# Optimization experiments

Hardware: AMD Instinct MI355X
Metric: run time of the kernel (lower is better)

Reference implementation:

```python
import jax, jax.numpy as jnp
import numpy as np

NEG_SLOPE_ATT = 0.2   # GATConv attention LeakyReLU
NEG_SLOPE_OUT = 0.01  # F.leaky_relu_ default on bend branch


def _gat(x, edge_index, edge_attr, W, a_src, a_dst, We, a_edge, bias):
    # Single-graph PyG GATConv (heads=1, concat=False, add_self_loops=True,
    # fill_value='mean' for self-loop edge_attr, dropout inactive in eval).
    # x: [N, F], edge_index: [2, E], edge_attr: [E, ED]
    N = x.shape[0]
    E = edge_attr.shape[0]
    h = x @ W  # [N, C] projected node features
    src, dst = edge_index[0], edge_index[1]
    # self-loop edge_attr = mean of incoming edge_attr per dst node
    deg = jax.ops.segment_sum(jnp.ones((E,), x.dtype), dst, num_segments=N)
    loop_attr = jax.ops.segment_sum(edge_attr, dst, num_segments=N) / jnp.maximum(deg, 1.0)[:, None]
    sl = jnp.arange(N)
    src2 = jnp.concatenate([src, sl])
    dst2 = jnp.concatenate([dst, sl])
    ea = jnp.concatenate([edge_attr, loop_attr], axis=0)  # [E+N, ED]
    eh = ea @ We  # [E+N, C]
    alpha = (h * a_src).sum(-1)[src2] + (h * a_dst).sum(-1)[dst2] + (eh * a_edge).sum(-1)
    alpha = jax.nn.leaky_relu(alpha, NEG_SLOPE_ATT)
    # per-dst-node softmax (stable)
    amax = jax.ops.segment_max(alpha, dst2, num_segments=N)
    ex = jnp.exp(alpha - amax[dst2])
    den = jax.ops.segment_sum(ex, dst2, num_segments=N)
    coef = ex / den[dst2]
    out = jax.ops.segment_sum(coef[:, None] * h[src2], dst2, num_segments=N)
    return out + bias


def setup_inputs() -> dict:
    key = jax.random.key(0)
    B, S, n, F, C, ED = 8, 16, 256, 128, 128, 4
    N = S * n
    Eb, Es = N * 16, n * 16
    ks = jax.random.split(key, 20)
    s = 0.1
    return {
        "x": jax.random.normal(ks[0], (B, S, n, F), jnp.float32),
        "section_edge_index": jax.random.randint(ks[1], (2, Es), 0, n),
        "bend_edge_index": jax.random.randint(ks[2], (2, Eb), 0, N),
        "section_edge_attr": jax.random.normal(ks[3], (B, Es, ED), jnp.float32),
        "bend_edge_attr": jax.random.normal(ks[4], (B, Eb, ED), jnp.float32),
        "enc_W": jax.random.normal(ks[5], (ED, ED), jnp.float32) * s,
        "enc_b": jnp.zeros((ED,), jnp.float32),
        "Wb": jax.random.normal(ks[6], (F, C), jnp.float32) * s,
        "a_src_b": jax.random.normal(ks[7], (C,), jnp.float32) * s,
        "a_dst_b": jax.random.normal(ks[8], (C,), jnp.float32) * s,
        "We_b": jax.random.normal(ks[9], (ED, C), jnp.float32) * s,
        "a_edge_b": jax.random.normal(ks[10], (C,), jnp.float32) * s,
        "bias_b": jnp.zeros((C,), jnp.float32),
        "Ws": jax.random.normal(ks[11], (F, C), jnp.float32) * s,
        "a_src_s": jax.random.normal(ks[12], (C,), jnp.float32) * s,
        "a_dst_s": jax.random.normal(ks[13], (C,), jnp.float32) * s,
        "We_s": jax.random.normal(ks[14], (ED, C), jnp.float32) * s,
        "a_edge_s": jax.random.normal(ks[15], (C,), jnp.float32) * s,
        "bias_s": jnp.zeros((C,), jnp.float32),
        "fuse_w": jnp.ones((2,), jnp.float32),
    }


def reference(x, section_edge_index, bend_edge_index, section_edge_attr, bend_edge_attr,
              enc_W, enc_b, Wb, a_src_b, a_dst_b, We_b, a_edge_b, bias_b,
              Ws, a_src_s, a_dst_s, We_s, a_edge_s, bias_s, fuse_w):
    B, S, n, F = x.shape
    enc_bend = bend_edge_attr @ enc_W + enc_b      # [B, Eb, ED]
    enc_sec = section_edge_attr @ enc_W + enc_b    # [B, Es, ED]
    # bend graph: one graph per batch element over all S*n nodes
    xb = x.reshape(B, S * n, F)
    gat_b = lambda xi, ei: _gat(xi, bend_edge_index, ei, Wb, a_src_b, a_dst_b, We_b, a_edge_b, bias_b)
    xb_out = jax.nn.leaky_relu(jax.vmap(gat_b)(xb, enc_bend), NEG_SLOPE_OUT)  # [B, S*n, C]
    # section graphs: one graph per (batch, section); edge_attr shared across sections
    es = jnp.broadcast_to(enc_sec[:, None], (B, S) + enc_sec.shape[1:]).reshape(B * S, *enc_sec.shape[1:])
    gat_s = lambda xi, ei: _gat(xi, section_edge_index, ei, Ws, a_src_s, a_dst_s, We_s, a_edge_s, bias_s)
    xs_out = jax.vmap(gat_s)(x.reshape(B * S, n, F), es).reshape(B, S * n, -1)
    w = jax.nn.softmax(fuse_w)
    return w[0] * xb_out + w[1] * xs_out
```

## Files before the change

kernel.cpp:

```cpp
#include <hip/hip_runtime.h>
#include <hip/hip_bf16.h>
#include <cstdint>
#include <cstddef>

#define NEG_ATT 0.2f
#define NEG_OUT 0.01f

constexpr int Bc = 8, Sc = 16, Nn = 256, Fd = 128, Cd = 128;
constexpr int NB = Sc * Nn;
constexpr int EB = NB * 16;
constexpr int ES = Nn * 16;
constexpr int NROWS = Bc * NB;
constexpr int CAP = 80;

constexpr size_t OFF_CONSTS = 0;
constexpr size_t OFF_WTB  = 4096;
constexpr size_t OFF_WTS  = OFF_WTB + (size_t)Fd * Cd * 2;
constexpr size_t OFF_HBP  = OFF_WTS + (size_t)Fd * Cd * 2;
constexpr size_t OFF_HSP  = OFF_HBP + (size_t)NROWS * 64 * 4;
constexpr size_t OFF_SSB  = OFF_HSP + (size_t)NROWS * 64 * 4;
constexpr size_t OFF_SDB  = OFF_SSB + (size_t)NROWS * 4;
constexpr size_t OFF_SSS  = OFF_SDB + (size_t)NROWS * 4;
constexpr size_t OFF_SDS  = OFF_SSS + (size_t)NROWS * 4;
constexpr size_t OFF_AEB  = OFF_SDS + (size_t)NROWS * 4;
constexpr size_t OFF_AES  = OFF_AEB + (size_t)Bc * EB * 4;
constexpr size_t OFF_ELLB = OFF_AES + (size_t)Bc * ES * 4;
constexpr size_t OFF_ELLS = OFF_ELLB + (size_t)NB * CAP * 4;
constexpr size_t OFF_FILB = OFF_ELLS + (size_t)Nn * CAP * 4;
constexpr size_t OFF_FILS = OFF_FILB + (size_t)NB * 4;
constexpr int ZERO_U32 = NB + Nn;


typedef short bf16x8 __attribute__((ext_vector_type(8)));
typedef float f32x4 __attribute__((ext_vector_type(4)));
#if defined(__has_builtin)
#if __has_builtin(__builtin_amdgcn_fdot2_f32_bf16)
#define HAS_DOT2BF 1
typedef __bf16 bf16x2 __attribute__((ext_vector_type(2)));
#endif
#endif

__device__ inline unsigned short f2bf(float f) {
  unsigned int u = __float_as_uint(f);
  u += 0x7fffu + ((u >> 16) & 1u);
  return (unsigned short)(u >> 16);
}
__device__ inline float lrelu(float x, float s) { return x > 0.f ? x : x * s; }
__device__ inline float bflo(unsigned int u) { return __uint_as_float(u << 16); }
__device__ inline float bfhi(unsigned int u) { return __uint_as_float(u & 0xffff0000u); }
__device__ inline float wave_dot128(const float* Wrow, const float* a, int lane) {
  float2 wv = *(const float2*)(Wrow + 2 * lane);
  float2 av = *(const float2*)(a + 2 * lane);
  float p = wv.x * av.x + wv.y * av.y;
  for (int off = 32; off; off >>= 1) p += __shfl_xor(p, off);
  return p;
}
__device__ inline void edge_fma(unsigned int u, uint4 v, float& o0, float& o1) {
#ifdef HAS_DOT2BF
  o0 = __builtin_amdgcn_fdot2_f32_bf16(__builtin_bit_cast(bf16x2, u),
                                       __builtin_bit_cast(bf16x2, v.y), o0, false);
  o1 = __builtin_amdgcn_fdot2_f32_bf16(__builtin_bit_cast(bf16x2, u),
                                       __builtin_bit_cast(bf16x2, v.z), o1, false);
#else
  float c = __uint_as_float(v.w);
  o0 += c * bflo(u); o1 += c * bfhi(u);
#endif
}

__global__ __launch_bounds__(256) void k_setup(
    const float* Wb, const float* a_src_b, const float* a_dst_b,
    const float* Ws, const float* a_src_s, const float* a_dst_s,
    const float* We_b, const float* a_edge_b,
    const float* We_s, const float* a_edge_s,
    const float* fuse_w, const float* enc_W, const float* enc_b,
    float* consts, unsigned short* wtb, unsigned short* wts, unsigned int* fill_region) {
  int blk = blockIdx.x, t = threadIdx.x;
  if (blk < 128) {
    int tid = blk * 256 + t;
    int which = tid >> 14, idx = tid & 16383;
    int c = idx >> 7, k = idx & 127;
    const float* W = which ? Ws : Wb;
    unsigned short* o = which ? wts : wtb;
    o[c * 128 + k] = f2bf(W[k * 128 + c]);
  } else if (blk < 160) {
    int wave = t >> 6, lane = t & 63;
    int gw = (blk - 128) * 4 + wave;
    int base = gw * 4;
    int v = base >> 7;
    const float* W = (v < 2) ? Wb : Ws;
    const float* a = (v == 0) ? a_src_b : (v == 1) ? a_dst_b : (v == 2) ? a_src_s : a_dst_s;
#pragma unroll
    for (int k = 0; k < 4; ++k) {
      int idx = base + k, f = idx & 127;
      float p = wave_dot128(W + f * 128, a, lane);
      if (lane == 0) consts[16 + v * 128 + f] = p;
    }
  } else if (blk == 160) {
    int wave = t >> 6, lane = t & 63;
    float pb = wave_dot128(We_b + wave * 128, a_edge_b, lane);
    float ps = wave_dot128(We_s + wave * 128, a_edge_s, lane);
    if (lane == 0) { consts[2 + wave] = pb; consts[6 + wave] = ps; }
    if (t == 0) {
      float f0 = fuse_w[0], f1 = fuse_w[1];
      float m = fmaxf(f0, f1);
      float e0 = __expf(f0 - m), e1 = __expf(f1 - m);
      consts[0] = e0 / (e0 + e1);
      consts[1] = e1 / (e0 + e1);
    }
  } else if (blk == 161) {
    if (t < 16) consts[544 + t] = enc_W[t];
    else if (t < 20) consts[544 + t] = enc_b[t - 16];
  } else {
    int zid = (blk - 162) * 256 + t;
    for (int z = zid; z < ZERO_U32; z += 2 * 256) fill_region[z] = 0;
  }
}

constexpr int GEMM_BLKS = NROWS / 64;
constexpr int ENC_BLKS  = (Bc * (EB + ES)) / 256;
constexpr int SCAT_BLKS = (EB + ES + 255) / 256;

__global__ __launch_bounds__(256) void k_work(
    const float* x, const float* consts,
    const unsigned short* wtb, const unsigned short* wts,
    unsigned int* hbp, unsigned int* hsp,
    float* ssb, float* sdb, float* sss, float* sds,
    const float* battr, const float* sattr, float* aeb, float* aes,
    const int* bsrc, const int* bdst, const int* ssrcA, const int* sdst,
    int* filb, int* fils, unsigned int* ellb, unsigned int* ells) {
  int blk = blockIdx.x, t = threadIdx.x;
  if (blk < GEMM_BLKS) {
    int wave = t >> 6, lane = t & 63;
    int m0 = blk * 64 + wave * 16;
    int r = lane & 15, kg = lane >> 4;
    f32x4 accB[8], accS[8];
#pragma unroll
    for (int i = 0; i < 8; ++i) { accB[i] = (f32x4){0,0,0,0}; accS[i] = (f32x4){0,0,0,0}; }
    float p0 = 0.f, p1 = 0.f, p2 = 0.f, p3 = 0.f;
    const float* wa = consts + 16;
#pragma unroll
    for (int ks = 0; ks < 4; ++ks) {
      int wo = ks * 32 + kg * 8;
      const float* xrow = x + (size_t)(m0 + r) * 128 + wo;
      float4 xa = *(const float4*)xrow;
      float4 xc = *(const float4*)(xrow + 4);
      float4 w0a = *(const float4*)(wa + 0 * 128 + wo), w0b = *(const float4*)(wa + 0 * 128 + wo + 4);
      float4 w1a = *(const float4*)(wa + 1 * 128 + wo), w1b = *(const float4*)(wa + 1 * 128 + wo + 4);
      float4 w2a = *(const float4*)(wa + 2 * 128 + wo), w2b = *(const float4*)(wa + 2 * 128 + wo + 4);
      float4 w3a = *(const float4*)(wa + 3 * 128 + wo), w3b = *(const float4*)(wa + 3 * 128 + wo + 4);
      p0 += xa.x*w0a.x + xa.y*w0a.y + xa.z*w0a.z + xa.w*w0a.w
          + xc.x*w0b.x + xc.y*w0b.y + xc.z*w0b.z + xc.w*w0b.w;
      p1 += xa.x*w1a.x + xa.y*w1a.y + xa.z*w1a.z + xa.w*w1a.w
          + xc.x*w1b.x + xc.y*w1b.y + xc.z*w1b.z + xc.w*w1b.w;
      p2 += xa.x*w2a.x + xa.y*w2a.y + xa.z*w2a.z + xa.w*w2a.w
          + xc.x*w2b.x + xc.y*w2b.y + xc.z*w2b.z + xc.w*w2b.w;
      p3 += xa.x*w3a.x + xa.y*w3a.y + xa.z*w3a.z + xa.w*w3a.w
          + xc.x*w3b.x + xc.y*w3b.y + xc.z*w3b.z + xc.w*w3b.w;
      bf16x8 a;
      a[0] = (short)f2bf(xa.x); a[1] = (short)f2bf(xa.y);
      a[2] = (short)f2bf(xa.z); a[3] = (short)f2bf(xa.w);
      a[4] = (short)f2bf(xc.x); a[5] = (short)f2bf(xc.y);
      a[6] = (short)f2bf(xc.z); a[7] = (short)f2bf(xc.w);
#pragma unroll
      for (int cb = 0; cb < 8; ++cb) {
        bf16x8 bb = *(const bf16x8*)(wtb + (size_t)(cb * 16 + r) * 128 + wo);
        accB[cb] = __builtin_amdgcn_mfma_f32_16x16x32_bf16(a, bb, accB[cb], 0, 0, 0);
        bf16x8 bs = *(const bf16x8*)(wts + (size_t)(cb * 16 + r) * 128 + wo);
        accS[cb] = __builtin_amdgcn_mfma_f32_16x16x32_bf16(a, bs, accS[cb], 0, 0, 0);
      }
    }
    p0 += __shfl_xor(p0, 16); p0 += __shfl_xor(p0, 32);
    p1 += __shfl_xor(p1, 16); p1 += __shfl_xor(p1, 32);
    p2 += __shfl_xor(p2, 16); p2 += __shfl_xor(p2, 32);
    p3 += __shfl_xor(p3, 16); p3 += __shfl_xor(p3, 32);
    if (lane < 16) {
      int row = m0 + lane;
      ssb[row] = p0; sdb[row] = p1; sss[row] = p2; sds[row] = p3;
    }
#pragma unroll
    for (int cb = 0; cb < 4; ++cb)
#pragma unroll
      for (int i = 0; i < 4; ++i) {
        size_t idx = (size_t)(m0 + kg * 4 + i) * 64 + cb * 16 + r;
        hbp[idx] = (unsigned int)f2bf(accB[cb][i]) | ((unsigned int)f2bf(accB[cb + 4][i]) << 16);
        hsp[idx] = (unsigned int)f2bf(accS[cb][i]) | ((unsigned int)f2bf(accS[cb + 4][i]) << 16);
      }
  } else if (blk < GEMM_BLKS + ENC_BLKS) {
    int idx = (blk - GEMM_BLKS) * 256 + t;
    const float* encW = consts + 544;
    bool isB = idx < Bc * EB;
    const float* attr = isB ? battr : sattr;
    const float* wae = consts + (isB ? 2 : 6);
    float* dst = isB ? aeb : aes;
    int id2 = isB ? idx : idx - Bc * EB;
    float4 at = *(const float4*)(attr + (size_t)id2 * 4);
    float e0 = encW[16] + at.x * encW[0] + at.y * encW[4] + at.z * encW[8]  + at.w * encW[12];
    float e1 = encW[17] + at.x * encW[1] + at.y * encW[5] + at.z * encW[9]  + at.w * encW[13];
    float e2 = encW[18] + at.x * encW[2] + at.y * encW[6] + at.z * encW[10] + at.w * encW[14];
    float e3 = encW[19] + at.x * encW[3] + at.y * encW[7] + at.z * encW[11] + at.w * encW[15];
    dst[id2] = e0 * wae[0] + e1 * wae[1] + e2 * wae[2] + e3 * wae[3];
  } else {
    int tid = (blk - GEMM_BLKS - ENC_BLKS) * 256 + t;
    if (tid < EB) {
      int d = bdst[tid];
      int slot = atomicAdd(&filb[d], 1);
      if (slot < CAP) ellb[(size_t)d * CAP + slot] = ((unsigned int)bsrc[tid] << 16) | (unsigned int)tid;
    } else if (tid < EB + ES) {
      int e = tid - EB;
      int d = sdst[e];
      int slot = atomicAdd(&fils[d], 1);
      if (slot < CAP) ells[(size_t)d * CAP + slot] = ((unsigned int)ssrcA[e] << 16) | (unsigned int)e;
    }
  }
}

__global__ __launch_bounds__(256) void k_gather(
    const float* ssb, const float* sdb, const float* aeb,
    const int* filb, const unsigned int* ellb, const unsigned int* hbp, const float* bias_b,
    const float* sss, const float* sds, const float* aes,
    const int* fils, const unsigned int* ells, const unsigned int* hsp, const float* bias_s,
    const float* consts, float* out) {
  __shared__ uint4 lds[4][128];
  int wg = blockIdx.x;
  int wave = threadIdx.x >> 6, lane = threadIdx.x & 63;
  int b = wg & 7;
  int i = ((wg >> 3) << 2) + wave;
  int wid = (b << 12) + i;
  int il = i & 255;
  int rowBase = wid - il;

  float oB0 = 0.f, oB1 = 0.f, oS0 = 0.f, oS1 = 0.f;

  int degB = filb[i];  if (degB > CAP) degB = CAP;
  int degS = fils[il]; if (degS > CAP) degS = CAP;
  const float* ssrcBb = ssb + ((size_t)b << 12);
  const float* ssrcGs = sss + rowBase;
  const float* aeBb = aeb + (size_t)b * EB;
  const float* aeBs = aes + (size_t)b * ES;
  const unsigned int* hBb = hbp + (((size_t)b << 12) << 6);
  const unsigned int* hGs = hsp + ((size_t)rowBase << 6);
  const unsigned int* ellBr = ellb + (size_t)i * CAP;
  const unsigned int* ellSr = ells + (size_t)il * CAP;
  unsigned int uSelfB = hbp[((size_t)wid << 6) + lane];
  unsigned int uSelfS = hsp[((size_t)wid << 6) + lane];
  float sdB = sdb[wid], sdS = sds[wid];
  float ssSelfB = ssrcBb[i], ssSelfS = ssrcGs[il];

  uint4* ldsw = lds[wave];

  if (degB <= 64 && degS <= 64) {
    bool vB = lane < degB, vS = lane < degS;
    unsigned int evB = vB ? ellBr[lane] : 0u;
    unsigned int evS = vS ? ellSr[lane] : 0u;
    int sB = evB >> 16, sS = evS >> 16;
    int eB = evB & 0xffffu, eS = evS & 0xffffu;
    float aevB = vB ? aeBb[eB] : 0.f;
    float aevS = vS ? aeBs[eS] : 0.f;
    float xsB = ssrcBb[sB];
    float xsS = ssrcGs[sS];

    float cB = vB ? __expf(lrelu(xsB + sdB + aevB, NEG_ATT)) : 0.f;
    float cS2 = vS ? __expf(lrelu(xsS + sdS + aevS, NEG_ATT)) : 0.f;

    float asumB = aevB, asumS = aevS, seB = cB, seS = cS2;
    for (int off = 32; off; off >>= 1) {
      asumB += __shfl_xor(asumB, off);
      asumS += __shfl_xor(asumS, off);
      seB += __shfl_xor(seB, off);
      seS += __shfl_xor(seS, off);
    }
    float aSB = lrelu(ssSelfB + sdB + asumB / (float)(degB > 0 ? degB : 1), NEG_ATT);
    float aSS = lrelu(ssSelfS + sdS + asumS / (float)(degS > 0 ? degS : 1), NEG_ATT);
    float eSB = __expf(aSB), eSS = __expf(aSS);
    float invB = 1.f / (seB + eSB);
    float invS = 1.f / (seS + eSS);

    {
      float cnB = cB * invB, cnS = cS2 * invS;
      unsigned int cb16 = (unsigned int)f2bf(cnB);
      unsigned int cs16 = (unsigned int)f2bf(cnS);
      uint4 slotB, slotS;
      slotB.x = (unsigned int)sB << 8; slotB.y = cb16; slotB.z = cb16 << 16; slotB.w = __float_as_uint(cnB);
      slotS.x = (unsigned int)sS << 8; slotS.y = cs16; slotS.z = cs16 << 16; slotS.w = __float_as_uint(cnS);
      ldsw[lane] = slotB;
      ldsw[64 + lane] = slotS;
    }

    const char* hBc = (const char*)hBb;
    const char* hGc = (const char*)hGs;
    int lb4 = lane * 4;
    int j = 0;
    for (; j + 4 <= degB; j += 4) {
      uint4 v0 = ldsw[j], v1 = ldsw[j+1], v2 = ldsw[j+2], v3 = ldsw[j+3];
      unsigned int u0 = *(const unsigned int*)(hBc + v0.x + lb4);
      unsigned int u1 = *(const unsigned int*)(hBc + v1.x + lb4);
      unsigned int u2 = *(const unsigned int*)(hBc + v2.x + lb4);
      unsigned int u3 = *(const unsigned int*)(hBc + v3.x + lb4);
      edge_fma(u0, v0, oB0, oB1); edge_fma(u1, v1, oB0, oB1);
      edge_fma(u2, v2, oB0, oB1); edge_fma(u3, v3, oB0, oB1);
    }
    for (; j < degB; ++j) {
      uint4 v = ldsw[j];
      unsigned int u = *(const unsigned int*)(hBc + v.x + lb4);
      edge_fma(u, v, oB0, oB1);
    }
    j = 0;
    for (; j + 4 <= degS; j += 4) {
      uint4 v0 = ldsw[64+j], v1 = ldsw[64+j+1], v2 = ldsw[64+j+2], v3 = ldsw[64+j+3];
      unsigned int u0 = *(const unsigned int*)(hGc + v0.x + lb4);
      unsigned int u1 = *(const unsigned int*)(hGc + v1.x + lb4);
      unsigned int u2 = *(const unsigned int*)(hGc + v2.x + lb4);
      unsigned int u3 = *(const unsigned int*)(hGc + v3.x + lb4);
      edge_fma(u0, v0, oS0, oS1); edge_fma(u1, v1, oS0, oS1);
      edge_fma(u2, v2, oS0, oS1); edge_fma(u3, v3, oS0, oS1);
    }
    for (; j < degS; ++j) {
      uint4 v = ldsw[64+j];
      unsigned int u = *(const unsigned int*)(hGc + v.x + lb4);
      edge_fma(u, v, oS0, oS1);
    }
    float cSelfB = eSB * invB;
    oB0 += cSelfB * bflo(uSelfB); oB1 += cSelfB * bfhi(uSelfB);
    float cSelfS = eSS * invS;
    oS0 += cSelfS * bflo(uSelfS); oS1 += cSelfS * bfhi(uSelfS);
  } else {
    float mB, invB, aSB, mS, invS, aSS;
    {
      float asum = 0.f;
      for (int p = lane; p < degB; p += 64) asum += aeBb[ellBr[p] & 0xffffu];
      for (int off = 32; off; off >>= 1) asum += __shfl_xor(asum, off);
      aSB = lrelu(ssSelfB + sdB + asum / (float)(degB > 0 ? degB : 1), NEG_ATT);
      mB = aSB;
      for (int p = lane; p < degB; p += 64) {
        unsigned int v = ellBr[p];
        mB = fmaxf(mB, lrelu(ssrcBb[v >> 16] + sdB + aeBb[v & 0xffffu], NEG_ATT));
      }
      for (int off = 32; off; off >>= 1) mB = fmaxf(mB, __shfl_xor(mB, off));
      float se = 0.f;
      for (int p = lane; p < degB; p += 64) {
        unsigned int v = ellBr[p];
        se += __expf(lrelu(ssrcBb[v >> 16] + sdB + aeBb[v & 0xffffu], NEG_ATT) - mB);
      }
      for (int off = 32; off; off >>= 1) se += __shfl_xor(se, off);
      se += __expf(aSB - mB);
      invB = 1.f / se;
      for (int j = 0; j < degB; ++j) {
        unsigned int v = ellBr[j];
        int s = v >> 16;
        float c = __expf(lrelu(ssrcBb[s] + sdB + aeBb[v & 0xffffu], NEG_ATT) - mB) * invB;
        unsigned int u = (hBb + ((size_t)s << 6))[lane];
        oB0 += c * bflo(u); oB1 += c * bfhi(u);
      }
      float cSelfB = __expf(aSB - mB) * invB;
      oB0 += cSelfB * bflo(uSelfB); oB1 += cSelfB * bfhi(uSelfB);
    }
    {
      float asum = 0.f;
      for (int p = lane; p < degS; p += 64) asum += aeBs[ellSr[p] & 0xffffu];
      for (int off = 32; off; off >>= 1) asum += __shfl_xor(asum, off);
      aSS = lrelu(ssSelfS + sdS + asum / (float)(degS > 0 ? degS : 1), NEG_ATT);
      mS = aSS;
      for (int p = lane; p < degS; p += 64) {
        unsigned int v = ellSr[p];
        mS = fmaxf(mS, lrelu(ssrcGs[v >> 16] + sdS + aeBs[v & 0xffffu], NEG_ATT));
      }
      for (int off = 32; off; off >>= 1) mS = fmaxf(mS, __shfl_xor(mS, off));
      float se = 0.f;
      for (int p = lane; p < degS; p += 64) {
        unsigned int v = ellSr[p];
        se += __expf(lrelu(ssrcGs[v >> 16] + sdS + aeBs[v & 0xffffu], NEG_ATT) - mS);
      }
      for (int off = 32; off; off >>= 1) se += __shfl_xor(se, off);
      se += __expf(aSS - mS);
      invS = 1.f / se;
      for (int j = 0; j < degS; ++j) {
        unsigned int v = ellSr[j];
        int s = v >> 16;
        float c = __expf(lrelu(ssrcGs[s] + sdS + aeBs[v & 0xffffu], NEG_ATT) - mS) * invS;
        unsigned int u = (hGs + ((size_t)s << 6))[lane];
        oS0 += c * bflo(u); oS1 += c * bfhi(u);
      }
      float cSelfS = __expf(aSS - mS) * invS;
      oS0 += cSelfS * bflo(uSelfS); oS1 += cSelfS * bfhi(uSelfS);
    }
  }

  float w0 = consts[0], w1 = consts[1];
  size_t o = (size_t)wid << 7;
  out[o + lane]      = w0 * lrelu(oB0 + bias_b[lane], NEG_OUT)      + w1 * (oS0 + bias_s[lane]);
  out[o + 64 + lane] = w0 * lrelu(oB1 + bias_b[lane + 64], NEG_OUT) + w1 * (oS1 + bias_s[lane + 64]);
}

extern "C" void kernel_launch(void* const* d_in, const int* in_sizes, int n_in,
                              void* d_out, int out_size, void* d_ws, size_t ws_size,
                              hipStream_t stream) {
  (void)in_sizes; (void)n_in; (void)out_size; (void)ws_size;
  const float* x        = (const float*)d_in[0];
  const int*   sec_ei   = (const int*)d_in[1];
  const int*   bend_ei  = (const int*)d_in[2];
  const float* sec_attr = (const float*)d_in[3];
  const float* bend_attr= (const float*)d_in[4];
  const float* enc_W    = (const float*)d_in[5];
  const float* enc_b    = (const float*)d_in[6];
  const float* Wb       = (const float*)d_in[7];
  const float* a_src_b  = (const float*)d_in[8];
  const float* a_dst_b  = (const float*)d_in[9];
  const float* We_b     = (const float*)d_in[10];
  const float* a_edge_b = (const float*)d_in[11];
  const float* bias_b   = (const float*)d_in[12];
  const float* Ws       = (const float*)d_in[13];
  const float* a_src_s  = (const float*)d_in[14];
  const float* a_dst_s  = (const float*)d_in[15];
  const float* We_s     = (const float*)d_in[16];
  const float* a_edge_s = (const float*)d_in[17];
  const float* bias_s   = (const float*)d_in[18];
  const float* fuse_w   = (const float*)d_in[19];
  float* out = (float*)d_out;

  char* ws = (char*)d_ws;
  float* consts = (float*)(ws + OFF_CONSTS);
  unsigned short* wtb = (unsigned short*)(ws + OFF_WTB);
  unsigned short* wts = (unsigned short*)(ws + OFF_WTS);
  unsigned int* hbp = (unsigned int*)(ws + OFF_HBP);
  unsigned int* hsp = (unsigned int*)(ws + OFF_HSP);
  float* ssb = (float*)(ws + OFF_SSB);
  float* sdb = (float*)(ws + OFF_SDB);
  float* sss = (float*)(ws + OFF_SSS);
  float* sds = (float*)(ws + OFF_SDS);
  float* aeb = (float*)(ws + OFF_AEB);
  float* aes = (float*)(ws + OFF_AES);
  unsigned int* ellb = (unsigned int*)(ws + OFF_ELLB);
  unsigned int* ells = (unsigned int*)(ws + OFF_ELLS);
  int* filb = (int*)(ws + OFF_FILB);
  int* fils = (int*)(ws + OFF_FILS);
  unsigned int* fill_region = (unsigned int*)(ws + OFF_FILB);

  const int* bend_src = bend_ei;
  const int* bend_dst = bend_ei + EB;
  const int* sec_src  = sec_ei;
  const int* sec_dst  = sec_ei + ES;

  k_setup<<<164, 256, 0, stream>>>(Wb, a_src_b, a_dst_b, Ws, a_src_s, a_dst_s,
                                   We_b, a_edge_b, We_s, a_edge_s, fuse_w,
                                   enc_W, enc_b, consts, wtb, wts, fill_region);

  k_work<<<GEMM_BLKS + ENC_BLKS + SCAT_BLKS, 256, 0, stream>>>(
      x, consts, wtb, wts, hbp, hsp, ssb, sdb, sss, sds,
      bend_attr, sec_attr, aeb, aes,
      bend_src, bend_dst, sec_src, sec_dst,
      filb, fils, ellb, ells);

  k_gather<<<NROWS / 4, 256, 0, stream>>>(ssb, sdb, aeb, filb, ellb, hbp, bias_b,
                                          sss, sds, aes, fils, ells, hsp, bias_s,
                                          consts, out);
}
```

Baseline: 69.79 us.

## Gather four edges per wave iteration with 16-byte loads per lane

The fast-path neighbour aggregation is restructured so each wave handles four edges per iteration. Each edge is split across 16 lanes, and each lane loads a 16-byte chunk of the bf16 feature row, replacing the old loop where every lane loaded 4 bytes for one edge at a time. The aim is to cut the serial gather iterations and load instructions and to keep more independent memory requests in flight. The cost is a cross-lane shuffle reduction at the end and more accumulator registers. The LDS slot shrinks to 8 bytes and carries an fp32 coefficient, which drops the bf16 fdot2 path, and the output is written as float4 from one lane group.

After: 72.49 us. 3.9% more time.

```diff
diff --git a/kernel.cpp b/kernel.cpp
--- a/kernel.cpp
+++ b/kernel.cpp
@@ -33,12 +33,6 @@
 
 typedef short bf16x8 __attribute__((ext_vector_type(8)));
 typedef float f32x4 __attribute__((ext_vector_type(4)));
-#if defined(__has_builtin)
-#if __has_builtin(__builtin_amdgcn_fdot2_f32_bf16)
-#define HAS_DOT2BF 1
-typedef __bf16 bf16x2 __attribute__((ext_vector_type(2)));
-#endif
-#endif
 
 __device__ inline unsigned short f2bf(float f) {
   unsigned int u = __float_as_uint(f);
@@ -54,17 +48,6 @@
   float p = wv.x * av.x + wv.y * av.y;
   for (int off = 32; off; off >>= 1) p += __shfl_xor(p, off);
   return p;
-}
-__device__ inline void edge_fma(unsigned int u, uint4 v, float& o0, float& o1) {
-#ifdef HAS_DOT2BF
-  o0 = __builtin_amdgcn_fdot2_f32_bf16(__builtin_bit_cast(bf16x2, u),
-                                       __builtin_bit_cast(bf16x2, v.y), o0, false);
-  o1 = __builtin_amdgcn_fdot2_f32_bf16(__builtin_bit_cast(bf16x2, u),
-                                       __builtin_bit_cast(bf16x2, v.z), o1, false);
-#else
-  float c = __uint_as_float(v.w);
-  o0 += c * bflo(u); o1 += c * bfhi(u);
-#endif
 }
 
 __global__ __launch_bounds__(256) void k_setup(
@@ -220,7 +203,7 @@
     const float* sss, const float* sds, const float* aes,
     const int* fils, const unsigned int* ells, const unsigned int* hsp, const float* bias_s,
     const float* consts, float* out) {
-  __shared__ uint4 lds[4][128];
+  __shared__ unsigned long long lds[4][128];
   int wg = blockIdx.x;
   int wave = threadIdx.x >> 6, lane = threadIdx.x & 63;
   int b = wg & 7;
@@ -228,8 +211,6 @@
   int wid = (b << 12) + i;
   int il = i & 255;
   int rowBase = wid - il;
-
-  float oB0 = 0.f, oB1 = 0.f, oS0 = 0.f, oS1 = 0.f;
 
   int degB = filb[i];  if (degB > CAP) degB = CAP;
   int degS = fils[il]; if (degS > CAP) degS = CAP;
@@ -241,12 +222,12 @@
   const unsigned int* hGs = hsp + ((size_t)rowBase << 6);
   const unsigned int* ellBr = ellb + (size_t)i * CAP;
   const unsigned int* ellSr = ells + (size_t)il * CAP;
-  unsigned int uSelfB = hbp[((size_t)wid << 6) + lane];
-  unsigned int uSelfS = hsp[((size_t)wid << 6) + lane];
   float sdB = sdb[wid], sdS = sds[wid];
   float ssSelfB = ssrcBb[i], ssSelfS = ssrcGs[il];
 
-  uint4* ldsw = lds[wave];
+  unsigned long long* ldsw = lds[wave];
+  float w0 = consts[0], w1 = consts[1];
+  size_t o = (size_t)wid << 7;
 
   if (degB <= 64 && degS <= 64) {
     bool vB = lane < degB, vS = lane < degS;
@@ -275,55 +256,77 @@
     float invB = 1.f / (seB + eSB);
     float invS = 1.f / (seS + eSS);
 
-    {
-      float cnB = cB * invB, cnS = cS2 * invS;
-      unsigned int cb16 = (unsigned int)f2bf(cnB);
-      unsigned int cs16 = (unsigned int)f2bf(cnS);
-      uint4 slotB, slotS;
-      slotB.x = (unsigned int)sB << 8; slotB.y = cb16; slotB.z = cb16 << 16; slotB.w = __float_as_uint(cnB);
-      slotS.x = (unsigned int)sS << 8; slotS.y = cs16; slotS.z = cs16 << 16; slotS.w = __float_as_uint(cnS);
-      ldsw[lane] = slotB;
-      ldsw[64 + lane] = slotS;
-    }
-
+    ldsw[lane]      = ((unsigned long long)__float_as_uint(cB * invB) << 32) | ((unsigned int)sB << 8);
+    ldsw[64 + lane] = ((unsigned long long)__float_as_uint(cS2 * invS) << 32) | ((unsigned int)sS << 8);
+
+    int g = lane >> 4, q = lane & 15;
+    int qb = q * 16;
     const char* hBc = (const char*)hBb;
     const char* hGc = (const char*)hGs;
-    int lb4 = lane * 4;
-    int j = 0;
-    for (; j + 4 <= degB; j += 4) {
-      uint4 v0 = ldsw[j], v1 = ldsw[j+1], v2 = ldsw[j+2], v3 = ldsw[j+3];
-      unsigned int u0 = *(const unsigned int*)(hBc + v0.x + lb4);
-      unsigned int u1 = *(const unsigned int*)(hBc + v1.x + lb4);
-      unsigned int u2 = *(const unsigned int*)(hBc + v2.x + lb4);
-      unsigned int u3 = *(const unsigned int*)(hBc + v3.x + lb4);
-      edge_fma(u0, v0, oB0, oB1); edge_fma(u1, v1, oB0, oB1);
-      edge_fma(u2, v2, oB0, oB1); edge_fma(u3, v3, oB0, oB1);
-    }
-    for (; j < degB; ++j) {
-      uint4 v = ldsw[j];
-      unsigned int u = *(const unsigned int*)(hBc + v.x + lb4);
-      edge_fma(u, v, oB0, oB1);
-    }
-    j = 0;
-    for (; j + 4 <= degS; j += 4) {
-      uint4 v0 = ldsw[64+j], v1 = ldsw[64+j+1], v2 = ldsw[64+j+2], v3 = ldsw[64+j+3];
-      unsigned int u0 = *(const unsigned int*)(hGc + v0.x + lb4);
-      unsigned int u1 = *(const unsigned int*)(hGc + v1.x + lb4);
-      unsigned int u2 = *(const unsigned int*)(hGc + v2.x + lb4);
-      unsigned int u3 = *(const unsigned int*)(hGc + v3.x + lb4);
-      edge_fma(u0, v0, oS0, oS1); edge_fma(u1, v1, oS0, oS1);
-      edge_fma(u2, v2, oS0, oS1); edge_fma(u3, v3, oS0, oS1);
-    }
-    for (; j < degS; ++j) {
-      uint4 v = ldsw[64+j];
-      unsigned int u = *(const unsigned int*)(hGc + v.x + lb4);
-      edge_fma(u, v, oS0, oS1);
-    }
-    float cSelfB = eSB * invB;
-    oB0 += cSelfB * bflo(uSelfB); oB1 += cSelfB * bfhi(uSelfB);
-    float cSelfS = eSS * invS;
-    oS0 += cSelfS * bflo(uSelfS); oS1 += cSelfS * bfhi(uSelfS);
+    float bLo0=0.f,bLo1=0.f,bLo2=0.f,bLo3=0.f, bHi0=0.f,bHi1=0.f,bHi2=0.f,bHi3=0.f;
+    float sLo0=0.f,sLo1=0.f,sLo2=0.f,sLo3=0.f, sHi0=0.f,sHi1=0.f,sHi2=0.f,sHi3=0.f;
+    for (int j = 0; j < degB; j += 4) {
+      unsigned long long v = ldsw[j + g];
+      uint4 u = *(const uint4*)(hBc + (unsigned int)v + qb);
+      float c = __uint_as_float((unsigned int)(v >> 32));
+      bLo0 += c * bflo(u.x); bHi0 += c * bfhi(u.x);
+      bLo1 += c * bflo(u.y); bHi1 += c * bfhi(u.y);
+      bLo2 += c * bflo(u.z); bHi2 += c * bfhi(u.z);
+      bLo3 += c * bflo(u.w); bHi3 += c * bfhi(u.w);
+    }
+    for (int j = 0; j < degS; j += 4) {
+      unsigned long long v = ldsw[64 + j + g];
+      uint4 u = *(const uint4*)(hGc + (unsigned int)v + qb);
+      float c = __uint_as_float((unsigned int)(v >> 32));
+      sLo0 += c * bflo(u.x); sHi0 += c * bfhi(u.x);
+      sLo1 += c * bflo(u.y); sHi1 += c * bfhi(u.y);
+      sLo2 += c * bflo(u.z); sHi2 += c * bfhi(u.z);
+      sLo3 += c * bflo(u.w); sHi3 += c * bfhi(u.w);
+    }
+    if (g == 0) {
+      float cfb = eSB * invB, cfs = eSS * invS;
+      uint4 ub = *(const uint4*)((const char*)hbp + ((size_t)wid << 8) + qb);
+      uint4 us = *(const uint4*)((const char*)hsp + ((size_t)wid << 8) + qb);
+      bLo0 += cfb * bflo(ub.x); bHi0 += cfb * bfhi(ub.x);
+      bLo1 += cfb * bflo(ub.y); bHi1 += cfb * bfhi(ub.y);
+      bLo2 += cfb * bflo(ub.z); bHi2 += cfb * bfhi(ub.z);
+      bLo3 += cfb * bflo(ub.w); bHi3 += cfb * bfhi(ub.w);
+      sLo0 += cfs * bflo(us.x); sHi0 += cfs * bfhi(us.x);
+      sLo1 += cfs * bflo(us.y); sHi1 += cfs * bfhi(us.y);
+      sLo2 += cfs * bflo(us.z); sHi2 += cfs * bfhi(us.z);
+      sLo3 += cfs * bflo(us.w); sHi3 += cfs * bfhi(us.w);
+    }
+    for (int off = 16; off <= 32; off <<= 1) {
+      bLo0 += __shfl_xor(bLo0, off); bLo1 += __shfl_xor(bLo1, off);
+      bLo2 += __shfl_xor(bLo2, off); bLo3 += __shfl_xor(bLo3, off);
+      bHi0 += __shfl_xor(bHi0, off); bHi1 += __shfl_xor(bHi1, off);
+      bHi2 += __shfl_xor(bHi2, off); bHi3 += __shfl_xor(bHi3, off);
+      sLo0 += __shfl_xor(sLo0, off); sLo1 += __shfl_xor(sLo1, off);
+      sLo2 += __shfl_xor(sLo2, off); sLo3 += __shfl_xor(sLo3, off);
+      sHi0 += __shfl_xor(sHi0, off); sHi1 += __shfl_xor(sHi1, off);
+      sHi2 += __shfl_xor(sHi2, off); sHi3 += __shfl_xor(sHi3, off);
+    }
+    if (g == 0) {
+      float4 bbL = *(const float4*)(bias_b + 4 * q);
+      float4 bbH = *(const float4*)(bias_b + 64 + 4 * q);
+      float4 bsL = *(const float4*)(bias_s + 4 * q);
+      float4 bsH = *(const float4*)(bias_s + 64 + 4 * q);
+      float4 r0, r1;
+      r0.x = w0 * lrelu(bLo0 + bbL.x, NEG_OUT) + w1 * (sLo0 + bsL.x);
+      r0.y = w0 * lrelu(bLo1 + bbL.y, NEG_OUT) + w1 * (sLo1 + bsL.y);
+      r0.z = w0 * lrelu(bLo2 + bbL.z, NEG_OUT) + w1 * (sLo2 + bsL.z);
+      r0.w = w0 * lrelu(bLo3 + bbL.w, NEG_OUT) + w1 * (sLo3 + bsL.w);
+      r1.x = w0 * lrelu(bHi0 + bbH.x, NEG_OUT) + w1 * (sHi0 + bsH.x);
+      r1.y = w0 * lrelu(bHi1 + bbH.y, NEG_OUT) + w1 * (sHi1 + bsH.y);
+      r1.z = w0 * lrelu(bHi2 + bbH.z, NEG_OUT) + w1 * (sHi2 + bsH.z);
+      r1.w = w0 * lrelu(bHi3 + bbH.w, NEG_OUT) + w1 * (sHi3 + bsH.w);
+      *(float4*)(out + o + 4 * q) = r0;
+      *(float4*)(out + o + 64 + 4 * q) = r1;
+    }
   } else {
+    float oB0 = 0.f, oB1 = 0.f, oS0 = 0.f, oS1 = 0.f;
+    unsigned int uSelfB = hbp[((size_t)wid << 6) + lane];
+    unsigned int uSelfS = hsp[((size_t)wid << 6) + lane];
     float mB, invB, aSB, mS, invS, aSS;
     {
       float asum = 0.f;
@@ -383,12 +386,9 @@
       float cSelfS = __expf(aSS - mS) * invS;
       oS0 += cSelfS * bflo(uSelfS); oS1 += cSelfS * bfhi(uSelfS);
     }
+    out[o + lane]      = w0 * lrelu(oB0 + bias_b[lane], NEG_OUT)      + w1 * (oS0 + bias_s[lane]);
+    out[o + 64 + lane] = w0 * lrelu(oB1 + bias_b[lane + 64], NEG_OUT) + w1 * (oS1 + bias_s[lane + 64]);
   }
-
-  float w0 = consts[0], w1 = consts[1];
-  size_t o = (size_t)wid << 7;
-  out[o + lane]      = w0 * lrelu(oB0 + bias_b[lane], NEG_OUT)      + w1 * (oS0 + bias_s[lane]);
-  out[o + 64 + lane] = w0 * lrelu(oB1 + bias_b[lane + 64], NEG_OUT) + w1 * (oS1 + bias_s[lane + 64]);
 }
 
 extern "C" void kernel_launch(void* const* d_in, const int* in_sizes, int n_in,
```

## Split bend and section aggregation across separate waves per node

Applied to the files above, without the earlier changes.

The gather kernel now gives each destination node two waves, one for the bend graph and one for the section graph, where before a single wave handled both. The section wave passes its partial result to the bend wave through LDS behind a block barrier, and the bend wave writes the fused output. The grid doubles to NROWS/2 blocks. The aim is more parallelism and shorter per-wave dependency chains for latency-bound gathers, at the cost of twice as many waves, a __syncthreads, and uneven work between the two waves of a node.

Measured after the change: 75.27 us. 1.08x slower.

```diff
diff --git a/kernel.cpp b/kernel.cpp
--- a/kernel.cpp
+++ b/kernel.cpp
@@ -220,175 +220,123 @@
     const float* sss, const float* sds, const float* aes,
     const int* fils, const unsigned int* ells, const unsigned int* hsp, const float* bias_s,
     const float* consts, float* out) {
-  __shared__ uint4 lds[4][128];
+  __shared__ uint4 slots[4][64];
+  __shared__ float cmb[2][128];
   int wg = blockIdx.x;
-  int wave = threadIdx.x >> 6, lane = threadIdx.x & 63;
+  int w = threadIdx.x >> 6, lane = threadIdx.x & 63;
   int b = wg & 7;
-  int i = ((wg >> 3) << 2) + wave;
+  int nl = w >> 1, ph = w & 1;
+  int i = ((wg >> 3) << 1) + nl;
   int wid = (b << 12) + i;
   int il = i & 255;
   int rowBase = wid - il;
 
-  float oB0 = 0.f, oB1 = 0.f, oS0 = 0.f, oS1 = 0.f;
-
-  int degB = filb[i];  if (degB > CAP) degB = CAP;
-  int degS = fils[il]; if (degS > CAP) degS = CAP;
-  const float* ssrcBb = ssb + ((size_t)b << 12);
-  const float* ssrcGs = sss + rowBase;
-  const float* aeBb = aeb + (size_t)b * EB;
-  const float* aeBs = aes + (size_t)b * ES;
-  const unsigned int* hBb = hbp + (((size_t)b << 12) << 6);
-  const unsigned int* hGs = hsp + ((size_t)rowBase << 6);
-  const unsigned int* ellBr = ellb + (size_t)i * CAP;
-  const unsigned int* ellSr = ells + (size_t)il * CAP;
-  unsigned int uSelfB = hbp[((size_t)wid << 6) + lane];
-  unsigned int uSelfS = hsp[((size_t)wid << 6) + lane];
-  float sdB = sdb[wid], sdS = sds[wid];
-  float ssSelfB = ssrcBb[i], ssSelfS = ssrcGs[il];
-
-  uint4* ldsw = lds[wave];
-
-  if (degB <= 64 && degS <= 64) {
-    bool vB = lane < degB, vS = lane < degS;
-    unsigned int evB = vB ? ellBr[lane] : 0u;
-    unsigned int evS = vS ? ellSr[lane] : 0u;
-    int sB = evB >> 16, sS = evS >> 16;
-    int eB = evB & 0xffffu, eS = evS & 0xffffu;
-    float aevB = vB ? aeBb[eB] : 0.f;
-    float aevS = vS ? aeBs[eS] : 0.f;
-    float xsB = ssrcBb[sB];
-    float xsS = ssrcGs[sS];
-
-    float cB = vB ? __expf(lrelu(xsB + sdB + aevB, NEG_ATT)) : 0.f;
-    float cS2 = vS ? __expf(lrelu(xsS + sdS + aevS, NEG_ATT)) : 0.f;
-
-    float asumB = aevB, asumS = aevS, seB = cB, seS = cS2;
+  float o0 = 0.f, o1 = 0.f;
+
+  const float* ssrc; const float* aeArr; const unsigned int* hB; const unsigned int* ellR;
+  int deg; float sd, ssSelf; int selfIdx;
+  if (ph == 0) {
+    deg = filb[i];  if (deg > CAP) deg = CAP;
+    ssrc = ssb + ((size_t)b << 12);
+    aeArr = aeb + (size_t)b * EB;
+    hB = hbp + (((size_t)b << 12) << 6);
+    ellR = ellb + (size_t)i * CAP;
+    sd = sdb[wid]; selfIdx = i;
+  } else {
+    deg = fils[il]; if (deg > CAP) deg = CAP;
+    ssrc = sss + rowBase;
+    aeArr = aes + (size_t)b * ES;
+    hB = hsp + ((size_t)rowBase << 6);
+    ellR = ells + (size_t)il * CAP;
+    sd = sds[wid]; selfIdx = il;
+  }
+  ssSelf = ssrc[selfIdx];
+  unsigned int uSelf = (ph == 0 ? hbp : hsp)[((size_t)wid << 6) + lane];
+  uint4* sl = slots[w];
+
+  if (deg <= 64) {
+    bool v = lane < deg;
+    unsigned int ev = v ? ellR[lane] : 0u;
+    int s = ev >> 16;
+    int e = ev & 0xffffu;
+    float aev = v ? aeArr[e] : 0.f;
+    float xs = ssrc[s];
+
+    float c = v ? __expf(lrelu(xs + sd + aev, NEG_ATT)) : 0.f;
+    float asum = aev, se = c;
     for (int off = 32; off; off >>= 1) {
-      asumB += __shfl_xor(asumB, off);
-      asumS += __shfl_xor(asumS, off);
-      seB += __shfl_xor(seB, off);
-      seS += __shfl_xor(seS, off);
-    }
-    float aSB = lrelu(ssSelfB + sdB + asumB / (float)(degB > 0 ? degB : 1), NEG_ATT);
-    float aSS = lrelu(ssSelfS + sdS + asumS / (float)(degS > 0 ? degS : 1), NEG_ATT);
-    float eSB = __expf(aSB), eSS = __expf(aSS);
-    float invB = 1.f / (seB + eSB);
-    float invS = 1.f / (seS + eSS);
-
+      asum += __shfl_xor(asum, off);
+      se += __shfl_xor(se, off);
+    }
+    float aS = lrelu(ssSelf + sd + asum / (float)(deg > 0 ? deg : 1), NEG_ATT);
+    float eS = __expf(aS);
+    float inv = 1.f / (se + eS);
+    float cn = c * inv;
     {
-      float cnB = cB * invB, cnS = cS2 * invS;
-      unsigned int cb16 = (unsigned int)f2bf(cnB);
-      unsigned int cs16 = (unsigned int)f2bf(cnS);
-      uint4 slotB, slotS;
-      slotB.x = (unsigned int)sB << 8; slotB.y = cb16; slotB.z = cb16 << 16; slotB.w = __float_as_uint(cnB);
-      slotS.x = (unsigned int)sS << 8; slotS.y = cs16; slotS.z = cs16 << 16; slotS.w = __float_as_uint(cnS);
-      ldsw[lane] = slotB;
-      ldsw[64 + lane] = slotS;
-    }
-
-    const char* hBc = (const char*)hBb;
-    const char* hGc = (const char*)hGs;
+      unsigned int c16 = (unsigned int)f2bf(cn);
+      uint4 slot;
+      slot.x = (unsigned int)s << 8; slot.y = c16; slot.z = c16 << 16; slot.w = __float_as_uint(cn);
+      sl[lane] = slot;
+    }
+    const char* hc = (const char*)hB;
     int lb4 = lane * 4;
     int j = 0;
-    for (; j + 4 <= degB; j += 4) {
-      uint4 v0 = ldsw[j], v1 = ldsw[j+1], v2 = ldsw[j+2], v3 = ldsw[j+3];
-      unsigned int u0 = *(const unsigned int*)(hBc + v0.x + lb4);
-      unsigned int u1 = *(const unsigned int*)(hBc + v1.x + lb4);
-      unsigned int u2 = *(const unsigned int*)(hBc + v2.x + lb4);
-      unsigned int u3 = *(const unsigned int*)(hBc + v3.x + lb4);
-      edge_fma(u0, v0, oB0, oB1); edge_fma(u1, v1, oB0, oB1);
-      edge_fma(u2, v2, oB0, oB1); edge_fma(u3, v3, oB0, oB1);
-    }
-    for (; j < degB; ++j) {
-      uint4 v = ldsw[j];
-      unsigned int u = *(const unsigned int*)(hBc + v.x + lb4);
-      edge_fma(u, v, oB0, oB1);
-    }
-    j = 0;
-    for (; j + 4 <= degS; j += 4) {
-      uint4 v0 = ldsw[64+j], v1 = ldsw[64+j+1], v2 = ldsw[64+j+2], v3 = ldsw[64+j+3];
-      unsigned int u0 = *(const unsigned int*)(hGc + v0.x + lb4);
-      unsigned int u1 = *(const unsigned int*)(hGc + v1.x + lb4);
-      unsigned int u2 = *(const unsigned int*)(hGc + v2.x + lb4);
-      unsigned int u3 = *(const unsigned int*)(hGc + v3.x + lb4);
-      edge_fma(u0, v0, oS0, oS1); edge_fma(u1, v1, oS0, oS1);
-      edge_fma(u2, v2, oS0, oS1); edge_fma(u3, v3, oS0, oS1);
-    }
-    for (; j < degS; ++j) {
-      uint4 v = ldsw[64+j];
-      unsigned int u = *(const unsigned int*)(hGc + v.x + lb4);
-      edge_fma(u, v, oS0, oS1);
-    }
-    float cSelfB = eSB * invB;
-    oB0 += cSelfB * bflo(uSelfB); oB1 += cSelfB * bfhi(uSelfB);
-    float cSelfS = eSS * invS;
-    oS0 += cSelfS * bflo(uSelfS); oS1 += cSelfS * bfhi(uSelfS);
+    for (; j + 4 <= deg; j += 4) {
+      uint4 v0 = sl[j], v1 = sl[j+1], v2 = sl[j+2], v3 = sl[j+3];
+      unsigned int u0 = *(const unsigned int*)(hc + v0.x + lb4);
+      unsigned int u1 = *(const unsigned int*)(hc + v1.x + lb4);
+      unsigned int u2 = *(const unsigned int*)(hc + v2.x + lb4);
+      unsigned int u3 = *(const unsigned int*)(hc + v3.x + lb4);
+      edge_fma(u0, v0, o0, o1); edge_fma(u1, v1, o0, o1);
+      edge_fma(u2, v2, o0, o1); edge_fma(u3, v3, o0, o1);
+    }
+    for (; j < deg; ++j) {
+      uint4 vv = sl[j];
+      unsigned int u = *(const unsigned int*)(hc + vv.x + lb4);
+      edge_fma(u, vv, o0, o1);
+    }
+    float cSelf = eS * inv;
+    o0 += cSelf * bflo(uSelf); o1 += cSelf * bfhi(uSelf);
   } else {
-    float mB, invB, aSB, mS, invS, aSS;
-    {
-      float asum = 0.f;
-      for (int p = lane; p < degB; p += 64) asum += aeBb[ellBr[p] & 0xffffu];
-      for (int off = 32; off; off >>= 1) asum += __shfl_xor(asum, off);
-      aSB = lrelu(ssSelfB + sdB + asum / (float)(degB > 0 ? degB : 1), NEG_ATT);
-      mB = aSB;
-      for (int p = lane; p < degB; p += 64) {
-        unsigned int v = ellBr[p];
-        mB = fmaxf(mB, lrelu(ssrcBb[v >> 16] + sdB + aeBb[v & 0xffffu], NEG_ATT));
-      }
-      for (int off = 32; off; off >>= 1) mB = fmaxf(mB, __shfl_xor(mB, off));
-      float se = 0.f;
-      for (int p = lane; p < degB; p += 64) {
-        unsigned int v = ellBr[p];
-        se += __expf(lrelu(ssrcBb[v >> 16] + sdB + aeBb[v & 0xffffu], NEG_ATT) - mB);
-      }
-      for (int off = 32; off; off >>= 1) se += __shfl_xor(se, off);
-      se += __expf(aSB - mB);
-      invB = 1.f / se;
-      for (int j = 0; j < degB; ++j) {
-        unsigned int v = ellBr[j];
-        int s = v >> 16;
-        float c = __expf(lrelu(ssrcBb[s] + sdB + aeBb[v & 0xffffu], NEG_ATT) - mB) * invB;
-        unsigned int u = (hBb + ((size_t)s << 6))[lane];
-        oB0 += c * bflo(u); oB1 += c * bfhi(u);
-      }
-      float cSelfB = __expf(aSB - mB) * invB;
-      oB0 += cSelfB * bflo(uSelfB); oB1 += cSelfB * bfhi(uSelfB);
-    }
-    {
-      float asum = 0.f;
-      for (int p = lane; p < degS; p += 64) asum += aeBs[ellSr[p] & 0xffffu];
-      for (int off = 32; off; off >>= 1) asum += __shfl_xor(asum, off);
-      aSS = lrelu(ssSelfS + sdS + asum / (float)(degS > 0 ? degS : 1), NEG_ATT);
-      mS = aSS;
-      for (int p = lane; p < degS; p += 64) {
-        unsigned int v = ellSr[p];
-        mS = fmaxf(mS, lrelu(ssrcGs[v >> 16] + sdS + aeBs[v & 0xffffu], NEG_ATT));
-      }
-      for (int off = 32; off; off >>= 1) mS = fmaxf(mS, __shfl_xor(mS, off));
-      float se = 0.f;
-      for (int p = lane; p < degS; p += 64) {
-        unsigned int v = ellSr[p];
-        se += __expf(lrelu(ssrcGs[v >> 16] + sdS + aeBs[v & 0xffffu], NEG_ATT) - mS);
-      }
-      for (int off = 32; off; off >>= 1) se += __shfl_xor(se, off);
-      se += __expf(aSS - mS);
-      invS = 1.f / se;
-      for (int j = 0; j < degS; ++j) {
-        unsigned int v = ellSr[j];
-        int s = v >> 16;
-        float c = __expf(lrelu(ssrcGs[s] + sdS + aeBs[v & 0xffffu], NEG_ATT) - mS) * invS;
-        unsigned int u = (hGs + ((size_t)s << 6))[lane];
-        oS0 += c * bflo(u); oS1 += c * bfhi(u);
-      }
-      float cSelfS = __expf(aSS - mS) * invS;
-      oS0 += cSelfS * bflo(uSelfS); oS1 += cSelfS * bfhi(uSelfS);
-    }
+    float asum = 0.f;
+    for (int p = lane; p < deg; p += 64) asum += aeArr[ellR[p] & 0xffffu];
+    for (int off = 32; off; off >>= 1) asum += __shfl_xor(asum, off);
+    float aS = lrelu(ssSelf + sd + asum / (float)(deg > 0 ? deg : 1), NEG_ATT);
+    float m = aS;
+    for (int p = lane; p < deg; p += 64) {
+      unsigned int v = ellR[p];
+      m = fmaxf(m, lrelu(ssrc[v >> 16] + sd + aeArr[v & 0xffffu], NEG_ATT));
+    }
+    for (int off = 32; off; off >>= 1) m = fmaxf(m, __shfl_xor(m, off));
+    float se = 0.f;
+    for (int p = lane; p < deg; p += 64) {
+      unsigned int v = ellR[p];
+      se += __expf(lrelu(ssrc[v >> 16] + sd + aeArr[v & 0xffffu], NEG_ATT) - m);
+    }
+    for (int off = 32; off; off >>= 1) se += __shfl_xor(se, off);
+    se += __expf(aS - m);
+    float inv = 1.f / se;
+    for (int j = 0; j < deg; ++j) {
+      unsigned int v = ellR[j];
+      int s = v >> 16;
+      float c = __expf(lrelu(ssrc[s] + sd + aeArr[v & 0xffffu], NEG_ATT) - m) * inv;
+      unsigned int u = (hB + ((size_t)s << 6))[lane];
+      o0 += c * bflo(u); o1 += c * bfhi(u);
+    }
+    float cSelf = __expf(aS - m) * inv;
+    o0 += cSelf * bflo(uSelf); o1 += cSelf * bfhi(uSelf);
   }
 
-  float w0 = consts[0], w1 = consts[1];
-  size_t o = (size_t)wid << 7;
-  out[o + lane]      = w0 * lrelu(oB0 + bias_b[lane], NEG_OUT)      + w1 * (oS0 + bias_s[lane]);
-  out[o + 64 + lane] = w0 * lrelu(oB1 + bias_b[lane + 64], NEG_OUT) + w1 * (oS1 + bias_s[lane + 64]);
+  if (ph == 1) { cmb[nl][lane] = o0; cmb[nl][64 + lane] = o1; }
+  __syncthreads();
+  if (ph == 0) {
+    float w0 = consts[0], w1 = consts[1];
+    size_t o = (size_t)wid << 7;
+    out[o + lane]      = w0 * lrelu(o0 + bias_b[lane], NEG_OUT)
+                       + w1 * (cmb[nl][lane] + bias_s[lane]);
+    out[o + 64 + lane] = w0 * lrelu(o1 + bias_b[lane + 64], NEG_OUT)
+                       + w1 * (cmb[nl][64 + lane] + bias_s[lane + 64]);
+  }
 }
 
 extern "C" void kernel_launch(void* const* d_in, const int* in_sizes, int n_in,
@@ -450,7 +398,7 @@
       bend_src, bend_dst, sec_src, sec_dst,
       filb, fils, ellb, ells);
 
-  k_gather<<<NROWS / 4, 256, 0, stream>>>(ssb, sdb, aeb, filb, ellb, hbp, bias_b,
+  k_gather<<<NROWS / 2, 256, 0, stream>>>(ssb, sdb, aeb, filb, ellb, hbp, bias_b,
                                           sss, sds, aes, fils, ells, hsp, bias_s,
                                           consts, out);
 }
```
